# Kernel tuning notes

Measured on AMD Instinct MI355X. Metric: run time of the kernel, lower is better.

## Reference

```python
import jax, jax.numpy as jnp
import numpy as np

T, B, OBS, H, A = 128, 256, 128, 512, 18
LSTM_IN = H + A + 1  # trunk_out + one_hot(a) + r


def setup_inputs() -> dict:
    key = jax.random.key(0)
    ks = jax.random.split(key, 24)

    def rn(k, shape, scale=0.05):
        return jax.random.normal(k, shape, dtype=jnp.float32) * scale

    inp = {
        "o": jax.random.normal(ks[0], (T, B, OBS), dtype=jnp.float32),
        "a": jax.random.randint(ks[1], (T, B), 0, A, dtype=jnp.int32),
        "r": jax.random.normal(ks[2], (T, B), dtype=jnp.float32),
        "done": (jax.random.uniform(ks[3], (T, B)) < 0.05).astype(jnp.float32),
        "h0": jax.random.normal(ks[4], (B, H), dtype=jnp.float32) * 0.1,
        "c0": jax.random.normal(ks[5], (B, H), dtype=jnp.float32) * 0.1,
        # trunk
        "tW0": rn(ks[6], (OBS, H)), "tb0": jnp.zeros((H,), jnp.float32),
        "tW1": rn(ks[7], (H, H)), "tb1": jnp.zeros((H,), jnp.float32),
        # LSTM (PyTorch layout: gates stacked as [i, f, g, o])
        "W_ih": rn(ks[8], (4 * H, LSTM_IN)), "W_hh": rn(ks[9], (4 * H, H)),
        "b_ih": jnp.zeros((4 * H,), jnp.float32), "b_hh": jnp.zeros((4 * H,), jnp.float32),
        # advantage head
        "aW0": rn(ks[10], (H, H)), "ab0": jnp.zeros((H,), jnp.float32),
        "aW1": rn(ks[11], (H, A)), "ab1": jnp.zeros((A,), jnp.float32),
        # value head
        "vW0": rn(ks[12], (H, H)), "vb0": jnp.zeros((H,), jnp.float32),
        "vW1": rn(ks[13], (H, 1)), "vb1": jnp.zeros((1,), jnp.float32),
    }
    return inp


def _forward(o, a, r, done, h0, c0, tW0, tb0, tW1, tb1,
             W_ih, W_hh, b_ih, b_hh, aW0, ab0, aW1, ab1, vW0, vb0, vW1, vb1):
    # shared trunk: two Linear+ReLU layers, vectorized over T*B
    hidden = jax.nn.relu(jnp.einsum('tbi,ih->tbh', o, tW0) + tb0)
    hidden = jax.nn.relu(jnp.einsum('tbi,ih->tbh', hidden, tW1) + tb1)
    a_oh = jax.nn.one_hot(a, A, dtype=jnp.float32)          # [T,B,A]
    x = jnp.concatenate([hidden, r[..., None], a_oh], -1)    # [T,B,LSTM_IN]

    # precompute input projection for all steps (not state-dependent)
    xg = jnp.einsum('tbi,gi->tbg', x, W_ih) + b_ih + b_hh    # [T,B,4H]

    def step(carry, inp):
        h, c = carry
        xg_t, d_t = inp
        keep = (1.0 - d_t)[:, None]                          # per-step done reset
        h, c = h * keep, c * keep
        gates = xg_t + h @ W_hh.T                            # [B,4H]
        i, f, g, og = jnp.split(gates, 4, axis=-1)
        c = jax.nn.sigmoid(f) * c + jax.nn.sigmoid(i) * jnp.tanh(g)
        h = jax.nn.sigmoid(og) * jnp.tanh(c)
        return (h, c), h

    (hT, cT), hs = jax.lax.scan(step, (h0, c0), (xg, done))  # hs: [T,B,H]

    ah = jax.nn.relu(jnp.einsum('tbh,hk->tbk', hs, aW0) + ab0)
    adv = jnp.einsum('tbk,ka->tba', ah, aW1) + ab1            # [T,B,A]
    vh = jax.nn.relu(jnp.einsum('tbh,hk->tbk', hs, vW0) + vb0)
    val = jnp.einsum('tbk,kv->tbv', vh, vW1) + vb1            # [T,B,1]
    q = val + (adv - adv.mean(axis=-1, keepdims=True))
    return q, hT, cT


def reference(o, a, r, done, h0, c0, tW0, tb0, tW1, tb1,
              W_ih, W_hh, b_ih, b_hh, aW0, ab0, aW1, ab1, vW0, vb0, vW1, vb1):
    return _forward(o, a, r, done, h0, c0, tW0, tb0, tW1, tb1,
                    W_ih, W_hh, b_ih, b_hh, aW0, ab0, aW1, ab1, vW0, vb0, vW1, vb1)
```

## Files before the change

### kernel.cpp

```cpp
#include <hip/hip_runtime.h>
#include <cstdint>

typedef unsigned short u16;
typedef unsigned int u32;
typedef unsigned long long u64;
typedef float f32x4 __attribute__((ext_vector_type(4)));
typedef short s16x8 __attribute__((ext_vector_type(8)));

#define DEV static __device__ __forceinline__

#define TT 128
#define BB 256
#define OBSD 128
#define HHD 512
#define AD 18
#define GGD 2048
#define MMD 32768

DEV u16 f2bf(float f) {
  u32 u = __builtin_bit_cast(u32, f);
  u += 0x7fffu + ((u >> 16) & 1u);
  return (u16)(u >> 16);
}
DEV float bf2f(u16 h) { return __builtin_bit_cast(float, ((u32)h) << 16); }

DEV f32x4 mfma16x16x32(s16x8 a, s16x8 b, f32x4 c) {
  asm("v_mfma_f32_16x16x32_bf16 %0, %1, %2, %0" : "+v"(c) : "v"(a), "v"(b));
  return c;
}
DEV void fence_mfma_read(f32x4& x) { asm volatile("s_nop 7" : "+v"(x)); }
DEV void fence_mfma_srcc(f32x4& x) { asm volatile("s_nop 1" : "+v"(x)); }

typedef __attribute__((address_space(3))) char lds_char;
typedef __attribute__((address_space(1))) const char gl_char;
DEV void gload16(const char* g, char* l) {
  __builtin_amdgcn_global_load_lds((const gl_char*)g, (lds_char*)l, 16, 0, 0);
}

DEV float sigm(float x) { return 1.f / (1.f + __expf(-x)); }
DEV float tanh_fast(float x) {
  float t = __expf(-2.f * fabsf(x));
  float r = (1.f - t) / (1.f + t);
  return copysignf(r, x);
}

constexpr size_t OFF_FLAGS = 0;
constexpr size_t OFF_HRING = 524288;
constexpr size_t OFF_TW0T  = 1048576;
constexpr size_t OFF_TW1T  = 1179648;
constexpr size_t OFF_AW0T  = 1703936;
constexpr size_t OFF_VW0T  = 2228224;
constexpr size_t OFF_AW1T  = 2752512;
constexpr size_t OFF_VW1T  = 2770944;
constexpr size_t OFF_WIH   = 2772992;
constexpr size_t OFF_WHH   = 4870144;
constexpr size_t OFF_BSUM  = 6967296;
constexpr size_t OFF_WRC   = 6975488;
constexpr size_t OFF_WEMB  = 6983680;
constexpr size_t OFF_BCAT  = 7131136;
constexpr size_t OFF_OBF   = 8388608;
constexpr size_t OFF_BUF1  = 16777216;
constexpr size_t OFF_BUF2  = 50331648;
constexpr size_t OFF_BUF3  = 83886080;

__global__ __launch_bounds__(256) void prep(
    const float* __restrict__ o, const float* __restrict__ tW0,
    const float* __restrict__ tW1, const float* __restrict__ aW0,
    const float* __restrict__ vW0, const float* __restrict__ aW1,
    const float* __restrict__ vW1, const float* __restrict__ Wih,
    const float* __restrict__ WhhF, const float* __restrict__ bih,
    const float* __restrict__ bhh, const float* __restrict__ h0,
    const float* __restrict__ done, const float* __restrict__ ab0,
    const float* __restrict__ vb0,
    u16* __restrict__ o_bf, u16* __restrict__ tW0T, u16* __restrict__ tW1T,
    u16* __restrict__ aW0T, u16* __restrict__ vW0T, u16* __restrict__ aW1T,
    u16* __restrict__ vW1T, u16* __restrict__ WihB, u16* __restrict__ WhhB,
    float* __restrict__ bsum, float* __restrict__ wrc, float* __restrict__ wemb,
    float* __restrict__ bcat, u16* __restrict__ hring)
{
  const int total = 4178432;
  for (int id = blockIdx.x * 256 + threadIdx.x; id < total; id += gridDim.x * 256) {
    int i = id;
    if (i < 1048576) {
      float4 v = ((const float4*)o)[i];
      u16* dst = o_bf + (size_t)i * 4;
      dst[0] = f2bf(v.x); dst[1] = f2bf(v.y); dst[2] = f2bf(v.z); dst[3] = f2bf(v.w);
      continue;
    }
    i -= 1048576;
    if (i < 65536)  { int n = i >> 7, k = i & 127; tW0T[i] = f2bf(tW0[k * 512 + n]); continue; }
    i -= 65536;
    if (i < 262144) { int n = i >> 9, k = i & 511; tW1T[i] = f2bf(tW1[k * 512 + n]); continue; }
    i -= 262144;
    if (i < 262144) { int n = i >> 9, k = i & 511; aW0T[i] = f2bf(aW0[k * 512 + n]); continue; }
    i -= 262144;
    if (i < 262144) { int n = i >> 9, k = i & 511; vW0T[i] = f2bf(vW0[k * 512 + n]); continue; }
    i -= 262144;
    if (i < 9216)   { int n = i >> 9, k = i & 511; aW1T[i] = f2bf(aW1[k * 18 + n]); continue; }
    i -= 9216;
    if (i < 512)    { vW1T[i] = f2bf(vW1[i]); continue; }
    i -= 512;
    if (i < 1048576){ int g = i >> 9, k = i & 511; WihB[i] = f2bf(Wih[g * 531 + k]); continue; }
    i -= 1048576;
    if (i < 1048576){ WhhB[i] = f2bf(WhhF[i]); continue; }
    i -= 1048576;
    if (i < 2048)   { bsum[i] = bih[i] + bhh[i]; wrc[i] = Wih[i * 531 + 512]; continue; }
    i -= 2048;
    if (i < 36864)  { int j = i >> 11, g = i & 2047; wemb[i] = Wih[g * 531 + 513 + j]; continue; }
    i -= 36864;
    if (i < 1024)   { bcat[i] = (i < 512) ? ab0[i] : vb0[i - 512]; continue; }
    i -= 1024;
    { int b = i >> 9; hring[i] = f2bf(h0[i] * (1.f - done[b])); }
  }
}

template<int MODE>
__global__ __launch_bounds__(256) void gemm_bt(
    const u16* __restrict__ A, const u16* __restrict__ Bt, u16* __restrict__ C,
    int Mdim, int Ndim, int Kdim,
    const float* __restrict__ bias,
    const float* __restrict__ wrc, const float* __restrict__ wemb,
    const float* __restrict__ rin, const int* __restrict__ ain)
{
  __shared__ __align__(16) char smem[32768];
  const int tid = threadIdx.x;
  const int nTn = Ndim >> 7;
  int wg = blockIdx.x;
  {
    const int per = gridDim.x >> 3;
    wg = (wg & 7) * per + (wg >> 3);
  }
  const int tm = wg / nTn, tn = wg % nTn;
  const int wid = tid >> 6, lane = tid & 63;
  const int wr = wid >> 1, wc = wid & 1;
  const int l15 = lane & 15, l4 = lane >> 4;

  f32x4 acc[4][4];
#pragma unroll
  for (int i = 0; i < 4; ++i)
#pragma unroll
    for (int j = 0; j < 4; ++j) acc[i][j] = f32x4{0.f, 0.f, 0.f, 0.f};

  const int srow = lane >> 3;
  const int scolb = ((lane & 7) * 16) ^ (srow << 4);
  const size_t kd2 = (size_t)Kdim * 2;
  const char* Abase = (const char*)(A + (size_t)tm * 128 * Kdim);
  const char* Bbase = (const char*)(Bt + (size_t)tn * 128 * Kdim);
  const char* ga[4]; const char* gb[4]; char* la[4]; char* lb[4];
#pragma unroll
  for (int j = 0; j < 4; ++j) {
    const int row = wid * 32 + j * 8 + srow;
    ga[j] = Abase + (size_t)row * kd2 + scolb;
    gb[j] = Bbase + (size_t)row * kd2 + scolb;
    la[j] = smem + wid * 4096 + j * 1024;
    lb[j] = smem + 16384 + wid * 4096 + j * 1024;
  }

  for (int k0 = 0; k0 < Kdim; k0 += 64) {
    const size_t kb = (size_t)k0 * 2;
#pragma unroll
    for (int j = 0; j < 4; ++j) {
      gload16(ga[j] + kb, la[j]);
      gload16(gb[j] + kb, lb[j]);
    }
    __syncthreads();
#pragma unroll
    for (int kk = 0; kk < 2; ++kk) {
      s16x8 af[4], bfr[4];
#pragma unroll
      for (int i = 0; i < 4; ++i) {
        int ar = wr * 64 + i * 16 + l15;
        af[i] = *(const s16x8*)(smem + ((ar * 128 + kk * 64 + l4 * 16) ^ ((ar & 7) << 4)));
        int br = wc * 64 + i * 16 + l15;
        bfr[i] = *(const s16x8*)(smem + 16384 + ((br * 128 + kk * 64 + l4 * 16) ^ ((br & 7) << 4)));
      }
#pragma unroll
      for (int i = 0; i < 4; ++i)
#pragma unroll
        for (int j = 0; j < 4; ++j)
          acc[i][j] = mfma16x16x32(af[i], bfr[j], acc[i][j]);
    }
    __syncthreads();
  }

#pragma unroll
  for (int i = 0; i < 4; ++i)
#pragma unroll
    for (int j = 0; j < 4; ++j) fence_mfma_read(acc[i][j]);

#pragma unroll
  for (int i = 0; i < 4; ++i) {
    const int rowb = tm * 128 + wr * 64 + i * 16 + l4 * 4;
    float rv[4]; int av[4];
    if (MODE == 1) {
#pragma unroll
      for (int r = 0; r < 4; ++r) { rv[r] = rin[rowb + r]; av[r] = ain[rowb + r]; }
    }
#pragma unroll
    for (int j = 0; j < 4; ++j) {
      const int col = tn * 128 + wc * 64 + j * 16 + l15;
      const float bs = bias[col];
      if (MODE == 0) {
#pragma unroll
        for (int r = 0; r < 4; ++r) {
          float x = acc[i][j][r] + bs;
          x = fmaxf(x, 0.f);
          C[(size_t)(rowb + r) * Ndim + col] = f2bf(x);
        }
      } else {
        const float wcv = wrc[col];
#pragma unroll
        for (int r = 0; r < 4; ++r) {
          float x = acc[i][j][r] + bs + rv[r] * wcv + wemb[av[r] * GGD + col];
          C[(size_t)(rowb + r) * Ndim + col] = f2bf(x);
        }
      }
    }
  }
}

__global__ __launch_bounds__(256) void lstm_seq(
    const u16* __restrict__ xg, const u16* __restrict__ WhhB,
    const float* __restrict__ done, const float* __restrict__ c0,
    u16* __restrict__ hring, u16* __restrict__ hs,
    float* __restrict__ hT, float* __restrict__ cT, u32* __restrict__ cnt)
{
  __shared__ __align__(16) char wsm[65536];
  const int tid = threadIdx.x;
  const int bg = blockIdx.x & 3;
  const int ug = blockIdx.x >> 2;
  const int b0 = bg * 64;
  const int u0 = ug * 16;

#pragma unroll
  for (int i = 0; i < 16; ++i) {
    int idx = i * 256 + tid;
    int lr = idx >> 6, c8 = idx & 63;
    int g = lr >> 4, uu = lr & 15;
    uint4 v = *(const uint4*)(WhhB + (size_t)(g * 512 + u0 + uu) * 512 + c8 * 8);
    *(uint4*)(wsm + ((lr * 1024 + c8 * 16) ^ ((lr & 7) << 4))) = v;
  }
  __syncthreads();

  const int wid = tid >> 6, lane = tid & 63;
  const int l15 = lane & 15, l4 = lane >> 4;
  const int mrow = wid * 16 + l4 * 4;
  const int afrow = b0 + wid * 16 + l15;
  const int u = u0 + l15;
  u32* const mycnt = cnt + ((bg << 2) | wid) * TT;

  float creg[4], kc[4], kn[4];
#pragma unroll
  for (int r = 0; r < 4; ++r) {
    creg[r] = c0[(size_t)(b0 + mrow + r) * HHD + u];
    kc[r] = 1.f - done[b0 + mrow + r];
    kn[r] = 1.f - done[BB + b0 + mrow + r];
  }

  u16 xpf[16];
#pragma unroll
  for (int g = 0; g < 4; ++g)
#pragma unroll
    for (int r = 0; r < 4; ++r)
      xpf[g * 4 + r] = xg[(size_t)(b0 + mrow + r) * GGD + g * HHD + u];

  for (int t = 0; t < TT; ++t) {
    const u16* hsrc = hring + (size_t)(t & 1) * (BB * HHD);
    u16* hdst = hring + (size_t)((t + 1) & 1) * (BB * HHD);

    f32x4 acc[4];
#pragma unroll
    for (int g = 0; g < 4; ++g)
#pragma unroll
      for (int r = 0; r < 4; ++r)
        acc[g][r] = bf2f(xpf[g * 4 + r]);
#pragma unroll
    for (int g = 0; g < 4; ++g) fence_mfma_srcc(acc[g]);

    u64 aflo[16], afhi[16];
    const u64* hb = (const u64*)(hsrc + (size_t)afrow * HHD);
#pragma unroll
    for (int kk = 0; kk < 16; ++kk) {
      aflo[kk] = __hip_atomic_load(hb + kk * 8 + l4 * 2,
                                   __ATOMIC_RELAXED, __HIP_MEMORY_SCOPE_AGENT);
      afhi[kk] = __hip_atomic_load(hb + kk * 8 + l4 * 2 + 1,
                                   __ATOMIC_RELAXED, __HIP_MEMORY_SCOPE_AGENT);
    }
#pragma unroll
    for (int kk = 0; kk < 16; ++kk) {
      union { u64 q[2]; s16x8 v; } tmp;
      tmp.q[0] = aflo[kk]; tmp.q[1] = afhi[kk];
      s16x8 a = tmp.v;
#pragma unroll
      for (int g = 0; g < 4; ++g) {
        int br = g * 16 + l15;
        s16x8 b = *(const s16x8*)(wsm + ((br * 1024 + kk * 64 + l4 * 16) ^ ((br & 7) << 4)));
        acc[g] = mfma16x16x32(a, b, acc[g]);
      }
    }
#pragma unroll
    for (int g = 0; g < 4; ++g) fence_mfma_read(acc[g]);

    float hv_[4], cv_[4];
#pragma unroll
    for (int r = 0; r < 4; ++r) {
      float iv = sigm(acc[0][r]);
      float fv = sigm(acc[1][r]);
      float gv = tanh_fast(acc[2][r]);
      float ov = sigm(acc[3][r]);
      float c = fv * (creg[r] * kc[r]) + iv * gv;
      float h = ov * tanh_fast(c);
      creg[r] = c; cv_[r] = c; hv_[r] = h;
    }

    if (t < TT - 1) {
      u32 pw[4];
#pragma unroll
      for (int r = 0; r < 4; ++r) {
        u16 ob = f2bf(hv_[r] * kn[r]);
        u16 pb = (u16)__shfl_xor((int)ob, 1, 64);
        pw[r] = ((l15 & 1) == 0) ? ((u32)ob | ((u32)pb << 16))
                                 : ((u32)pb | ((u32)ob << 16));
      }
      {
        const int rb = (l15 & 1) * 2;
        u32* hd32 = (u32*)hdst;
        const int col2 = (u0 + (l15 & ~1)) >> 1;
        __hip_atomic_store(&hd32[(size_t)(b0 + mrow + rb) * 256 + col2], pw[rb],
                           __ATOMIC_RELAXED, __HIP_MEMORY_SCOPE_AGENT);
        __hip_atomic_store(&hd32[(size_t)(b0 + mrow + rb + 1) * 256 + col2], pw[rb + 1],
                           __ATOMIC_RELAXED, __HIP_MEMORY_SCOPE_AGENT);
      }
      asm volatile("s_waitcnt vmcnt(0)" ::: "memory");
      if (lane == 0)
        __hip_atomic_fetch_add(&mycnt[t], 1u,
                               __ATOMIC_RELAXED, __HIP_MEMORY_SCOPE_AGENT);
#pragma unroll
      for (int r = 0; r < 4; ++r)
        hs[((size_t)t * BB + b0 + mrow + r) * HHD + u] = f2bf(hv_[r]);
#pragma unroll
      for (int g = 0; g < 4; ++g)
#pragma unroll
        for (int r = 0; r < 4; ++r)
          xpf[g * 4 + r] = xg[((size_t)(t + 1) * BB + b0 + mrow + r) * GGD + g * HHD + u];
#pragma unroll
      for (int r = 0; r < 4; ++r) {
        kc[r] = kn[r];
        kn[r] = (t + 2 < TT) ? (1.f - done[(size_t)(t + 2) * BB + b0 + mrow + r]) : 1.f;
      }
      while (__hip_atomic_load(&mycnt[t],
                               __ATOMIC_RELAXED, __HIP_MEMORY_SCOPE_AGENT) < 32u)
        __builtin_amdgcn_s_sleep(1);
    } else {
#pragma unroll
      for (int r = 0; r < 4; ++r) {
        hs[((size_t)t * BB + b0 + mrow + r) * HHD + u] = f2bf(hv_[r]);
        hT[(size_t)(b0 + mrow + r) * HHD + u] = hv_[r];
        cT[(size_t)(b0 + mrow + r) * HHD + u] = cv_[r];
      }
    }
  }
}

__global__ __launch_bounds__(256) void head_final(
    const u16* __restrict__ hv, const u16* __restrict__ aW1T,
    const u16* __restrict__ vW1T, const float* __restrict__ ab1,
    const float* __restrict__ vb1, float* __restrict__ q)
{
  __shared__ __align__(16) u16 wa[AD * HHD];
  __shared__ __align__(16) u16 wv[HHD];
  const int tid = threadIdx.x;
  for (int i = tid; i < AD * HHD / 8; i += 256) ((uint4*)wa)[i] = ((const uint4*)aW1T)[i];
  for (int i = tid; i < HHD / 8; i += 256) ((uint4*)wv)[i] = ((const uint4*)vW1T)[i];
  __syncthreads();
  const int wid = tid >> 6, lane = tid & 63;
  for (int row = blockIdx.x * 4 + wid; row < MMD; row += gridDim.x * 4) {
    uint4 va = *(const uint4*)(hv + (size_t)row * 1024 + lane * 8);
    uint4 vv = *(const uint4*)(hv + (size_t)row * 1024 + 512 + lane * 8);
    const u16* pa = (const u16*)&va;
    const u16* pv = (const u16*)&vv;
    float af[8], vf[8];
#pragma unroll
    for (int j = 0; j < 8; ++j) { af[j] = bf2f(pa[j]); vf[j] = bf2f(pv[j]); }
    float accs[19];
#pragma unroll
    for (int n = 0; n < 19; ++n) accs[n] = 0.f;
#pragma unroll
    for (int n = 0; n < AD; ++n) {
      const u16* w = wa + n * HHD + lane * 8;
#pragma unroll
      for (int j = 0; j < 8; ++j) accs[n] += af[j] * bf2f(w[j]);
    }
    {
      const u16* w = wv + lane * 8;
#pragma unroll
      for (int j = 0; j < 8; ++j) accs[18] += vf[j] * bf2f(w[j]);
    }
#pragma unroll
    for (int n = 0; n < 19; ++n) {
#pragma unroll
      for (int off = 32; off > 0; off >>= 1)
        accs[n] += __shfl_xor(accs[n], off, 64);
    }
    if (lane == 0) {
      float s = 0.f;
      float advv[AD];
#pragma unroll
      for (int n = 0; n < AD; ++n) { advv[n] = accs[n] + ab1[n]; s += advv[n]; }
      float val = accs[18] + vb1[0];
      float mean = s * (1.f / 18.f);
#pragma unroll
      for (int n = 0; n < AD; ++n) q[(size_t)row * AD + n] = val + advv[n] - mean;
    }
  }
}

extern "C" void kernel_launch(void* const* d_in, const int* in_sizes, int n_in,
                              void* d_out, int out_size, void* d_ws, size_t ws_size,
                              hipStream_t stream) {
  const float* o    = (const float*)d_in[0];
  const int*   a    = (const int*)d_in[1];
  const float* r    = (const float*)d_in[2];
  const float* done = (const float*)d_in[3];
  const float* h0   = (const float*)d_in[4];
  const float* c0   = (const float*)d_in[5];
  const float* tW0  = (const float*)d_in[6];
  const float* tb0  = (const float*)d_in[7];
  const float* tW1  = (const float*)d_in[8];
  const float* tb1  = (const float*)d_in[9];
  const float* Wih  = (const float*)d_in[10];
  const float* Whh  = (const float*)d_in[11];
  const float* bih  = (const float*)d_in[12];
  const float* bhh  = (const float*)d_in[13];
  const float* aW0  = (const float*)d_in[14];
  const float* ab0  = (const float*)d_in[15];
  const float* aW1  = (const float*)d_in[16];
  const float* ab1  = (const float*)d_in[17];
  const float* vW0  = (const float*)d_in[18];
  const float* vb0  = (const float*)d_in[19];
  const float* vW1  = (const float*)d_in[20];
  const float* vb1  = (const float*)d_in[21];
  (void)in_sizes; (void)n_in; (void)ws_size;

  char* ws = (char*)d_ws;
  u32* cnt    = (u32*)(ws + OFF_FLAGS);
  u16* hring  = (u16*)(ws + OFF_HRING);
  u16* tW0T   = (u16*)(ws + OFF_TW0T);
  u16* tW1T   = (u16*)(ws + OFF_TW1T);
  u16* aW0T   = (u16*)(ws + OFF_AW0T);
  u16* vW0T   = (u16*)(ws + OFF_VW0T);
  u16* aW1T   = (u16*)(ws + OFF_AW1T);
  u16* vW1T   = (u16*)(ws + OFF_VW1T);
  u16* WihB   = (u16*)(ws + OFF_WIH);
  u16* WhhB   = (u16*)(ws + OFF_WHH);
  float* bsum = (float*)(ws + OFF_BSUM);
  float* wrc  = (float*)(ws + OFF_WRC);
  float* wemb = (float*)(ws + OFF_WEMB);
  float* bcat = (float*)(ws + OFF_BCAT);
  u16* o_bf   = (u16*)(ws + OFF_OBF);
  u16* buf1   = (u16*)(ws + OFF_BUF1);
  u16* buf2   = (u16*)(ws + OFF_BUF2);
  u16* buf3   = (u16*)(ws + OFF_BUF3);

  float* qout = (float*)d_out;
  float* hT   = qout + (size_t)TT * BB * AD;
  float* cT   = hT + (size_t)BB * HHD;

  hipMemsetAsync(cnt, 0, 65536, stream);
  prep<<<2048, 256, 0, stream>>>(o, tW0, tW1, aW0, vW0, aW1, vW1, Wih, Whh,
                                 bih, bhh, h0, done, ab0, vb0,
                                 o_bf, tW0T, tW1T, aW0T, vW0T, aW1T, vW1T,
                                 WihB, WhhB, bsum, wrc, wemb, bcat, hring);
  gemm_bt<0><<<1024, 256, 0, stream>>>(o_bf, tW0T, buf1, MMD, 512, 128, tb0,
                                       nullptr, nullptr, nullptr, nullptr);
  gemm_bt<0><<<1024, 256, 0, stream>>>(buf1, tW1T, buf2, MMD, 512, 512, tb1,
                                       nullptr, nullptr, nullptr, nullptr);
  gemm_bt<1><<<4096, 256, 0, stream>>>(buf2, WihB, buf3, MMD, 2048, 512, bsum,
                                       wrc, wemb, r, a);
  lstm_seq<<<128, 256, 0, stream>>>(buf3, WhhB, done, c0, hring,
                                    buf1 , hT, cT, cnt);
  gemm_bt<0><<<2048, 256, 0, stream>>>(buf1 , aW0T, buf3 , MMD, 1024, 512, bcat,
                                       nullptr, nullptr, nullptr, nullptr);
  head_final<<<2048, 256, 0, stream>>>(buf3, aW1T, vW1T, ab1, vb1, qout);
}
```

Measured before the change: 1.122 ms.

## Shrink LSTM grid to 32 blocks with per-row-group slot flags

The persistent LSTM kernel now runs on 32 blocks instead of 128. Each block owns 16 hidden units across all 256 batch rows, and each wave walks four row-group chunks per step. The single shared atomic counter per row group is replaced by per-producer slot flags, which a wave polls with a ballot before loading the previous h, and the xg prefetch moves ahead of the MFMA loop. The aim is to cut cross-block synchronization cost and let chunks pipeline, at the price of four times more serial work per block and fewer CUs in use.

```diff
diff --git a/kernel.cpp b/kernel.cpp
--- a/kernel.cpp
+++ b/kernel.cpp
@@ -219,17 +219,15 @@
   }
 }
 
-__global__ __launch_bounds__(256) void lstm_seq(
+__global__ __launch_bounds__(256, 1) void lstm_seq(
     const u16* __restrict__ xg, const u16* __restrict__ WhhB,
     const float* __restrict__ done, const float* __restrict__ c0,
     u16* __restrict__ hring, u16* __restrict__ hs,
-    float* __restrict__ hT, float* __restrict__ cT, u32* __restrict__ cnt)
+    float* __restrict__ hT, float* __restrict__ cT, u32* __restrict__ slots)
 {
   __shared__ __align__(16) char wsm[65536];
   const int tid = threadIdx.x;
-  const int bg = blockIdx.x & 3;
-  const int ug = blockIdx.x >> 2;
-  const int b0 = bg * 64;
+  const int ug = blockIdx.x;
   const int u0 = ug * 16;
 
 #pragma unroll
@@ -244,119 +242,140 @@
 
   const int wid = tid >> 6, lane = tid & 63;
   const int l15 = lane & 15, l4 = lane >> 4;
-  const int mrow = wid * 16 + l4 * 4;
-  const int afrow = b0 + wid * 16 + l15;
   const int u = u0 + l15;
-  u32* const mycnt = cnt + ((bg << 2) | wid) * TT;
-
-  float creg[4], kc[4], kn[4];
-#pragma unroll
-  for (int r = 0; r < 4; ++r) {
-    creg[r] = c0[(size_t)(b0 + mrow + r) * HHD + u];
-    kc[r] = 1.f - done[b0 + mrow + r];
-    kn[r] = 1.f - done[BB + b0 + mrow + r];
-  }
-
-  u16 xpf[16];
-#pragma unroll
-  for (int g = 0; g < 4; ++g)
-#pragma unroll
-    for (int r = 0; r < 4; ++r)
-      xpf[g * 4 + r] = xg[(size_t)(b0 + mrow + r) * GGD + g * HHD + u];
+
+  float creg[4][4], kc[4][4], kn[4][4];
+  u16 xpf[4][16];
+#pragma unroll
+  for (int ch = 0; ch < 4; ++ch) {
+    const int b0 = (ch * 4 + wid) * 16;
+#pragma unroll
+    for (int r = 0; r < 4; ++r) {
+      const int row = b0 + l4 * 4 + r;
+      creg[ch][r] = c0[(size_t)row * HHD + u];
+      kc[ch][r] = 1.f - done[row];
+      kn[ch][r] = 1.f - done[BB + row];
+    }
+#pragma unroll
+    for (int g = 0; g < 4; ++g)
+#pragma unroll
+      for (int r = 0; r < 4; ++r)
+        xpf[ch][g * 4 + r] = xg[(size_t)(b0 + l4 * 4 + r) * GGD + g * HHD + u];
+  }
 
   for (int t = 0; t < TT; ++t) {
     const u16* hsrc = hring + (size_t)(t & 1) * (BB * HHD);
     u16* hdst = hring + (size_t)((t + 1) & 1) * (BB * HHD);
 
-    f32x4 acc[4];
-#pragma unroll
-    for (int g = 0; g < 4; ++g)
-#pragma unroll
-      for (int r = 0; r < 4; ++r)
-        acc[g][r] = bf2f(xpf[g * 4 + r]);
-#pragma unroll
-    for (int g = 0; g < 4; ++g) fence_mfma_srcc(acc[g]);
-
-    u64 aflo[16], afhi[16];
-    const u64* hb = (const u64*)(hsrc + (size_t)afrow * HHD);
-#pragma unroll
-    for (int kk = 0; kk < 16; ++kk) {
-      aflo[kk] = __hip_atomic_load(hb + kk * 8 + l4 * 2,
-                                   __ATOMIC_RELAXED, __HIP_MEMORY_SCOPE_AGENT);
-      afhi[kk] = __hip_atomic_load(hb + kk * 8 + l4 * 2 + 1,
-                                   __ATOMIC_RELAXED, __HIP_MEMORY_SCOPE_AGENT);
-    }
-#pragma unroll
-    for (int kk = 0; kk < 16; ++kk) {
-      union { u64 q[2]; s16x8 v; } tmp;
-      tmp.q[0] = aflo[kk]; tmp.q[1] = afhi[kk];
-      s16x8 a = tmp.v;
-#pragma unroll
-      for (int g = 0; g < 4; ++g) {
-        int br = g * 16 + l15;
-        s16x8 b = *(const s16x8*)(wsm + ((br * 1024 + kk * 64 + l4 * 16) ^ ((br & 7) << 4)));
-        acc[g] = mfma16x16x32(a, b, acc[g]);
-      }
-    }
-#pragma unroll
-    for (int g = 0; g < 4; ++g) fence_mfma_read(acc[g]);
-
-    float hv_[4], cv_[4];
-#pragma unroll
-    for (int r = 0; r < 4; ++r) {
-      float iv = sigm(acc[0][r]);
-      float fv = sigm(acc[1][r]);
-      float gv = tanh_fast(acc[2][r]);
-      float ov = sigm(acc[3][r]);
-      float c = fv * (creg[r] * kc[r]) + iv * gv;
-      float h = ov * tanh_fast(c);
-      creg[r] = c; cv_[r] = c; hv_[r] = h;
-    }
-
-    if (t < TT - 1) {
-      u32 pw[4];
+#pragma unroll
+    for (int ch = 0; ch < 4; ++ch) {
+      const int rg = ch * 4 + wid;
+      const int b0 = rg * 16;
+      const int mrow = l4 * 4;
+
+      if (t > 0) {
+        for (;;) {
+          u32 v = 1;
+          if (lane < 32)
+            v = __hip_atomic_load(&slots[((size_t)rg * TT + (t - 1)) * 32 + lane],
+                                  __ATOMIC_RELAXED, __HIP_MEMORY_SCOPE_AGENT);
+          if (__all(v != 0)) break;
+          __builtin_amdgcn_s_sleep(1);
+        }
+      }
+
+      u64 aflo[16], afhi[16];
+      const u64* hb = (const u64*)(hsrc + (size_t)(b0 + l15) * HHD);
+#pragma unroll
+      for (int kk = 0; kk < 16; ++kk) {
+        aflo[kk] = __hip_atomic_load(hb + kk * 8 + l4 * 2,
+                                     __ATOMIC_RELAXED, __HIP_MEMORY_SCOPE_AGENT);
+        afhi[kk] = __hip_atomic_load(hb + kk * 8 + l4 * 2 + 1,
+                                     __ATOMIC_RELAXED, __HIP_MEMORY_SCOPE_AGENT);
+      }
+
+      f32x4 acc[4];
+#pragma unroll
+      for (int g = 0; g < 4; ++g)
+#pragma unroll
+        for (int r = 0; r < 4; ++r)
+          acc[g][r] = bf2f(xpf[ch][g * 4 + r]);
+#pragma unroll
+      for (int g = 0; g < 4; ++g) fence_mfma_srcc(acc[g]);
+
+      if (t < TT - 1) {
+#pragma unroll
+        for (int g = 0; g < 4; ++g)
+#pragma unroll
+          for (int r = 0; r < 4; ++r)
+            xpf[ch][g * 4 + r] =
+                xg[((size_t)(t + 1) * BB + b0 + mrow + r) * GGD + g * HHD + u];
+      }
+
+#pragma unroll
+      for (int kk = 0; kk < 16; ++kk) {
+        union { u64 q[2]; s16x8 v; } tmp;
+        tmp.q[0] = aflo[kk]; tmp.q[1] = afhi[kk];
+        s16x8 a = tmp.v;
+#pragma unroll
+        for (int g = 0; g < 4; ++g) {
+          int br = g * 16 + l15;
+          s16x8 b = *(const s16x8*)(wsm + ((br * 1024 + kk * 64 + l4 * 16) ^ ((br & 7) << 4)));
+          acc[g] = mfma16x16x32(a, b, acc[g]);
+        }
+      }
+#pragma unroll
+      for (int g = 0; g < 4; ++g) fence_mfma_read(acc[g]);
+
+      float hv_[4], cv_[4];
 #pragma unroll
       for (int r = 0; r < 4; ++r) {
-        u16 ob = f2bf(hv_[r] * kn[r]);
-        u16 pb = (u16)__shfl_xor((int)ob, 1, 64);
-        pw[r] = ((l15 & 1) == 0) ? ((u32)ob | ((u32)pb << 16))
-                                 : ((u32)pb | ((u32)ob << 16));
-      }
-      {
-        const int rb = (l15 & 1) * 2;
-        u32* hd32 = (u32*)hdst;
-        const int col2 = (u0 + (l15 & ~1)) >> 1;
-        __hip_atomic_store(&hd32[(size_t)(b0 + mrow + rb) * 256 + col2], pw[rb],
-                           __ATOMIC_RELAXED, __HIP_MEMORY_SCOPE_AGENT);
-        __hip_atomic_store(&hd32[(size_t)(b0 + mrow + rb + 1) * 256 + col2], pw[rb + 1],
-                           __ATOMIC_RELAXED, __HIP_MEMORY_SCOPE_AGENT);
-      }
-      asm volatile("s_waitcnt vmcnt(0)" ::: "memory");
-      if (lane == 0)
-        __hip_atomic_fetch_add(&mycnt[t], 1u,
-                               __ATOMIC_RELAXED, __HIP_MEMORY_SCOPE_AGENT);
-#pragma unroll
-      for (int r = 0; r < 4; ++r)
-        hs[((size_t)t * BB + b0 + mrow + r) * HHD + u] = f2bf(hv_[r]);
-#pragma unroll
-      for (int g = 0; g < 4; ++g)
+        float iv = sigm(acc[0][r]);
+        float fv = sigm(acc[1][r]);
+        float gv = tanh_fast(acc[2][r]);
+        float ov = sigm(acc[3][r]);
+        float c = fv * (creg[ch][r] * kc[ch][r]) + iv * gv;
+        float h = ov * tanh_fast(c);
+        creg[ch][r] = c; cv_[r] = c; hv_[r] = h;
+      }
+
+      if (t < TT - 1) {
 #pragma unroll
         for (int r = 0; r < 4; ++r)
-          xpf[g * 4 + r] = xg[((size_t)(t + 1) * BB + b0 + mrow + r) * GGD + g * HHD + u];
-#pragma unroll
-      for (int r = 0; r < 4; ++r) {
-        kc[r] = kn[r];
-        kn[r] = (t + 2 < TT) ? (1.f - done[(size_t)(t + 2) * BB + b0 + mrow + r]) : 1.f;
-      }
-      while (__hip_atomic_load(&mycnt[t],
-                               __ATOMIC_RELAXED, __HIP_MEMORY_SCOPE_AGENT) < 32u)
-        __builtin_amdgcn_s_sleep(1);
-    } else {
-#pragma unroll
-      for (int r = 0; r < 4; ++r) {
-        hs[((size_t)t * BB + b0 + mrow + r) * HHD + u] = f2bf(hv_[r]);
-        hT[(size_t)(b0 + mrow + r) * HHD + u] = hv_[r];
-        cT[(size_t)(b0 + mrow + r) * HHD + u] = cv_[r];
+          hs[((size_t)t * BB + b0 + mrow + r) * HHD + u] = f2bf(hv_[r]);
+        u32 pw[4];
+#pragma unroll
+        for (int r = 0; r < 4; ++r) {
+          u16 ob = f2bf(hv_[r] * kn[ch][r]);
+          u16 pb = (u16)__shfl_xor((int)ob, 1, 64);
+          pw[r] = ((l15 & 1) == 0) ? ((u32)ob | ((u32)pb << 16))
+                                   : ((u32)pb | ((u32)ob << 16));
+        }
+        {
+          const int rb = (l15 & 1) * 2;
+          u32* hd32 = (u32*)hdst;
+          const int col2 = (u0 + (l15 & ~1)) >> 1;
+          __hip_atomic_store(&hd32[(size_t)(b0 + mrow + rb) * 256 + col2], pw[rb],
+                             __ATOMIC_RELAXED, __HIP_MEMORY_SCOPE_AGENT);
+          __hip_atomic_store(&hd32[(size_t)(b0 + mrow + rb + 1) * 256 + col2], pw[rb + 1],
+                             __ATOMIC_RELAXED, __HIP_MEMORY_SCOPE_AGENT);
+        }
+        asm volatile("s_waitcnt vmcnt(0)" ::: "memory");
+        if (lane == 0)
+          __hip_atomic_store(&slots[((size_t)rg * TT + t) * 32 + ug], 1u,
+                             __ATOMIC_RELAXED, __HIP_MEMORY_SCOPE_AGENT);
+#pragma unroll
+        for (int r = 0; r < 4; ++r) {
+          kc[ch][r] = kn[ch][r];
+          kn[ch][r] = (t + 2 < TT) ? (1.f - done[(size_t)(t + 2) * BB + b0 + mrow + r]) : 1.f;
+        }
+      } else {
+#pragma unroll
+        for (int r = 0; r < 4; ++r) {
+          hs[((size_t)t * BB + b0 + mrow + r) * HHD + u] = f2bf(hv_[r]);
+          hT[(size_t)(b0 + mrow + r) * HHD + u] = hv_[r];
+          cT[(size_t)(b0 + mrow + r) * HHD + u] = cv_[r];
+        }
       }
     }
   }
@@ -443,7 +462,7 @@
   (void)in_sizes; (void)n_in; (void)ws_size;
 
   char* ws = (char*)d_ws;
-  u32* cnt    = (u32*)(ws + OFF_FLAGS);
+  u32* slots  = (u32*)(ws + OFF_FLAGS);
   u16* hring  = (u16*)(ws + OFF_HRING);
   u16* tW0T   = (u16*)(ws + OFF_TW0T);
   u16* tW1T   = (u16*)(ws + OFF_TW1T);
@@ -466,7 +485,7 @@
   float* hT   = qout + (size_t)TT * BB * AD;
   float* cT   = hT + (size_t)BB * HHD;
 
-  hipMemsetAsync(cnt, 0, 65536, stream);
+  hipMemsetAsync(slots, 0, 262144, stream);
   prep<<<2048, 256, 0, stream>>>(o, tW0, tW1, aW0, vW0, aW1, vW1, Wih, Whh,
                                  bih, bhh, h0, done, ab0, vb0,
                                  o_bf, tW0T, tW1T, aW0T, vW0T, aW1T, vW1T,
@@ -477,8 +496,8 @@
                                        nullptr, nullptr, nullptr, nullptr);
   gemm_bt<1><<<4096, 256, 0, stream>>>(buf2, WihB, buf3, MMD, 2048, 512, bsum,
                                        wrc, wemb, r, a);
-  lstm_seq<<<128, 256, 0, stream>>>(buf3, WhhB, done, c0, hring,
-                                    buf1 , hT, cT, cnt);
+  lstm_seq<<<32, 256, 0, stream>>>(buf3, WhhB, done, c0, hring,
+                                   buf1 , hT, cT, slots);
   gemm_bt<0><<<2048, 256, 0, stream>>>(buf1 , aW0T, buf3 , MMD, 1024, 512, bcat,
                                        nullptr, nullptr, nullptr, nullptr);
   head_final<<<2048, 256, 0, stream>>>(buf3, aW1T, vW1T, ab1, vb1, qout);
```

After: 3.943 ms. +251.4%, slower.

## Fuse head first-layer GEMM into LSTM recurrence using idle per-step compute

Applied to the files above, without the earlier changes.

Moves the advantage/value head's first Linear+ReLU into the persistent LSTM kernel. Each step it multiplies the previous step's h fragments, already held in registers, by a 32-column slice of the head weights kept in LDS, and writes the ah/vh outputs directly. This removes the separate head GEMM launch and the hs write/read round trip. Done-masking moves from scaling h at store time to masking the A-fragments at load, so the unmasked h can be reused by the head. The trade-off is extra MFMA work, 32KB more LDS per block, and more stores on the latency-critical serial path.

```diff
diff --git a/kernel.cpp b/kernel.cpp
--- a/kernel.cpp
+++ b/kernel.cpp
@@ -30,6 +30,7 @@
 }
 DEV void fence_mfma_read(f32x4& x) { asm volatile("s_nop 7" : "+v"(x)); }
 DEV void fence_mfma_srcc(f32x4& x) { asm volatile("s_nop 1" : "+v"(x)); }
+DEV void fence_valu_srca(s16x8& x) { asm volatile("s_nop 1" : "+v"(x)); }
 
 typedef __attribute__((address_space(3))) char lds_char;
 typedef __attribute__((address_space(1))) const char gl_char;
@@ -70,8 +71,7 @@
     const float* __restrict__ vW1, const float* __restrict__ Wih,
     const float* __restrict__ WhhF, const float* __restrict__ bih,
     const float* __restrict__ bhh, const float* __restrict__ h0,
-    const float* __restrict__ done, const float* __restrict__ ab0,
-    const float* __restrict__ vb0,
+    const float* __restrict__ ab0, const float* __restrict__ vb0,
     u16* __restrict__ o_bf, u16* __restrict__ tW0T, u16* __restrict__ tW1T,
     u16* __restrict__ aW0T, u16* __restrict__ vW0T, u16* __restrict__ aW1T,
     u16* __restrict__ vW1T, u16* __restrict__ WihB, u16* __restrict__ WhhB,
@@ -110,7 +110,7 @@
     i -= 36864;
     if (i < 1024)   { bcat[i] = (i < 512) ? ab0[i] : vb0[i - 512]; continue; }
     i -= 1024;
-    { int b = i >> 9; hring[i] = f2bf(h0[i] * (1.f - done[b])); }
+    { hring[i] = f2bf(h0[i]); }
   }
 }
 
@@ -219,18 +219,21 @@
   }
 }
 
-__global__ __launch_bounds__(256) void lstm_seq(
+__global__ __launch_bounds__(256, 1) void lstm_seq(
     const u16* __restrict__ xg, const u16* __restrict__ WhhB,
-    const float* __restrict__ done, const float* __restrict__ c0,
-    u16* __restrict__ hring, u16* __restrict__ hs,
+    const u16* __restrict__ WheadT, const float* __restrict__ done,
+    const float* __restrict__ c0, const float* __restrict__ bcat,
+    u16* __restrict__ hring, u16* __restrict__ ah, u16* __restrict__ vh,
     float* __restrict__ hT, float* __restrict__ cT, u32* __restrict__ cnt)
 {
   __shared__ __align__(16) char wsm[65536];
+  __shared__ __align__(16) char whd[32768];
   const int tid = threadIdx.x;
   const int bg = blockIdx.x & 3;
   const int ug = blockIdx.x >> 2;
   const int b0 = bg * 64;
   const int u0 = ug * 16;
+  const int hc0 = ug * 32;
 
 #pragma unroll
   for (int i = 0; i < 16; ++i) {
@@ -240,6 +243,13 @@
     uint4 v = *(const uint4*)(WhhB + (size_t)(g * 512 + u0 + uu) * 512 + c8 * 8);
     *(uint4*)(wsm + ((lr * 1024 + c8 * 16) ^ ((lr & 7) << 4))) = v;
   }
+#pragma unroll
+  for (int i = 0; i < 8; ++i) {
+    int idx = i * 256 + tid;
+    int lr = idx >> 6, c8 = idx & 63;
+    uint4 v = *(const uint4*)(WheadT + (size_t)(hc0 + lr) * 512 + c8 * 8);
+    *(uint4*)(whd + ((lr * 1024 + c8 * 16) ^ ((lr & 7) << 4))) = v;
+  }
   __syncthreads();
 
   const int wid = tid >> 6, lane = tid & 63;
@@ -249,13 +259,20 @@
   const int u = u0 + l15;
   u32* const mycnt = cnt + ((bg << 2) | wid) * TT;
 
-  float creg[4], kc[4], kn[4];
+  u16* const hvout = (ug < 16) ? ah : vh;
+  const int hcl = (ug < 16) ? hc0 : hc0 - 512;
+  float bcv[2];
+#pragma unroll
+  for (int j = 0; j < 2; ++j) bcv[j] = bcat[hc0 + j * 16 + l15];
+
+  float creg[4], kc[4];
 #pragma unroll
   for (int r = 0; r < 4; ++r) {
     creg[r] = c0[(size_t)(b0 + mrow + r) * HHD + u];
     kc[r] = 1.f - done[b0 + mrow + r];
-    kn[r] = 1.f - done[BB + b0 + mrow + r];
-  }
+  }
+  u64 am;
+  { float dn = done[afrow]; am = (dn != 0.f) ? 0ull : ~0ull; }
 
   u16 xpf[16];
 #pragma unroll
@@ -289,8 +306,9 @@
 #pragma unroll
     for (int kk = 0; kk < 16; ++kk) {
       union { u64 q[2]; s16x8 v; } tmp;
-      tmp.q[0] = aflo[kk]; tmp.q[1] = afhi[kk];
+      tmp.q[0] = aflo[kk] & am; tmp.q[1] = afhi[kk] & am;
       s16x8 a = tmp.v;
+      fence_valu_srca(a);
 #pragma unroll
       for (int g = 0; g < 4; ++g) {
         int br = g * 16 + l15;
@@ -313,59 +331,129 @@
       creg[r] = c; cv_[r] = c; hv_[r] = h;
     }
 
-    if (t < TT - 1) {
+    {
       u32 pw[4];
 #pragma unroll
       for (int r = 0; r < 4; ++r) {
-        u16 ob = f2bf(hv_[r] * kn[r]);
+        u16 ob = f2bf(hv_[r]);
         u16 pb = (u16)__shfl_xor((int)ob, 1, 64);
         pw[r] = ((l15 & 1) == 0) ? ((u32)ob | ((u32)pb << 16))
                                  : ((u32)pb | ((u32)ob << 16));
       }
-      {
-        const int rb = (l15 & 1) * 2;
-        u32* hd32 = (u32*)hdst;
-        const int col2 = (u0 + (l15 & ~1)) >> 1;
-        __hip_atomic_store(&hd32[(size_t)(b0 + mrow + rb) * 256 + col2], pw[rb],
-                           __ATOMIC_RELAXED, __HIP_MEMORY_SCOPE_AGENT);
-        __hip_atomic_store(&hd32[(size_t)(b0 + mrow + rb + 1) * 256 + col2], pw[rb + 1],
-                           __ATOMIC_RELAXED, __HIP_MEMORY_SCOPE_AGENT);
-      }
-      asm volatile("s_waitcnt vmcnt(0)" ::: "memory");
-      if (lane == 0)
-        __hip_atomic_fetch_add(&mycnt[t], 1u,
-                               __ATOMIC_RELAXED, __HIP_MEMORY_SCOPE_AGENT);
-#pragma unroll
-      for (int r = 0; r < 4; ++r)
-        hs[((size_t)t * BB + b0 + mrow + r) * HHD + u] = f2bf(hv_[r]);
+      const int rb = (l15 & 1) * 2;
+      u32* hd32 = (u32*)hdst;
+      const int col2 = (u0 + (l15 & ~1)) >> 1;
+      __hip_atomic_store(&hd32[(size_t)(b0 + mrow + rb) * 256 + col2], pw[rb],
+                         __ATOMIC_RELAXED, __HIP_MEMORY_SCOPE_AGENT);
+      __hip_atomic_store(&hd32[(size_t)(b0 + mrow + rb + 1) * 256 + col2], pw[rb + 1],
+                         __ATOMIC_RELAXED, __HIP_MEMORY_SCOPE_AGENT);
+    }
+    asm volatile("s_waitcnt vmcnt(0)" ::: "memory");
+    if (lane == 0)
+      __hip_atomic_fetch_add(&mycnt[t], 1u,
+                             __ATOMIC_RELAXED, __HIP_MEMORY_SCOPE_AGENT);
+
+    if (t > 0) {
+      f32x4 acch[2];
+#pragma unroll
+      for (int j = 0; j < 2; ++j)
+#pragma unroll
+        for (int r = 0; r < 4; ++r) acch[j][r] = bcv[j];
+#pragma unroll
+      for (int j = 0; j < 2; ++j) fence_mfma_srcc(acch[j]);
+#pragma unroll
+      for (int kk = 0; kk < 16; ++kk) {
+        union { u64 q[2]; s16x8 v; } tmp;
+        tmp.q[0] = aflo[kk]; tmp.q[1] = afhi[kk];
+        s16x8 a = tmp.v;
+#pragma unroll
+        for (int j = 0; j < 2; ++j) {
+          int br = j * 16 + l15;
+          s16x8 b = *(const s16x8*)(whd + ((br * 1024 + kk * 64 + l4 * 16) ^ ((br & 7) << 4)));
+          acch[j] = mfma16x16x32(a, b, acch[j]);
+        }
+      }
+#pragma unroll
+      for (int j = 0; j < 2; ++j) fence_mfma_read(acch[j]);
+#pragma unroll
+      for (int j = 0; j < 2; ++j)
+#pragma unroll
+        for (int r = 0; r < 4; ++r) {
+          float x = fmaxf(acch[j][r], 0.f);
+          hvout[((size_t)(t - 1) * BB + b0 + mrow + r) * 512 + hcl + j * 16 + l15] = f2bf(x);
+        }
+    }
+    if (t == TT - 1) {
+#pragma unroll
+      for (int r = 0; r < 4; ++r) {
+        hT[(size_t)(b0 + mrow + r) * HHD + u] = hv_[r];
+        cT[(size_t)(b0 + mrow + r) * HHD + u] = cv_[r];
+      }
+    } else {
 #pragma unroll
       for (int g = 0; g < 4; ++g)
 #pragma unroll
         for (int r = 0; r < 4; ++r)
           xpf[g * 4 + r] = xg[((size_t)(t + 1) * BB + b0 + mrow + r) * GGD + g * HHD + u];
 #pragma unroll
+      for (int r = 0; r < 4; ++r)
+        kc[r] = 1.f - done[(size_t)(t + 1) * BB + b0 + mrow + r];
+      float dn = done[(size_t)(t + 1) * BB + afrow];
+      am = (dn != 0.f) ? 0ull : ~0ull;
+    }
+
+    while (__hip_atomic_load(&mycnt[t],
+                             __ATOMIC_RELAXED, __HIP_MEMORY_SCOPE_AGENT) < 32u)
+      __builtin_amdgcn_s_sleep(1);
+  }
+
+  {
+    const u16* hfin = hring + (size_t)(TT & 1) * (BB * HHD);
+    u64 aflo[16], afhi[16];
+    const u64* hb = (const u64*)(hfin + (size_t)afrow * HHD);
+#pragma unroll
+    for (int kk = 0; kk < 16; ++kk) {
+      aflo[kk] = __hip_atomic_load(hb + kk * 8 + l4 * 2,
+                                   __ATOMIC_RELAXED, __HIP_MEMORY_SCOPE_AGENT);
+      afhi[kk] = __hip_atomic_load(hb + kk * 8 + l4 * 2 + 1,
+                                   __ATOMIC_RELAXED, __HIP_MEMORY_SCOPE_AGENT);
+    }
+    f32x4 acch[2];
+#pragma unroll
+    for (int j = 0; j < 2; ++j)
+#pragma unroll
+      for (int r = 0; r < 4; ++r) acch[j][r] = bcv[j];
+#pragma unroll
+    for (int j = 0; j < 2; ++j) fence_mfma_srcc(acch[j]);
+#pragma unroll
+    for (int kk = 0; kk < 16; ++kk) {
+      union { u64 q[2]; s16x8 v; } tmp;
+      tmp.q[0] = aflo[kk]; tmp.q[1] = afhi[kk];
+      s16x8 a = tmp.v;
+#pragma unroll
+      for (int j = 0; j < 2; ++j) {
+        int br = j * 16 + l15;
+        s16x8 b = *(const s16x8*)(whd + ((br * 1024 + kk * 64 + l4 * 16) ^ ((br & 7) << 4)));
+        acch[j] = mfma16x16x32(a, b, acch[j]);
+      }
+    }
+#pragma unroll
+    for (int j = 0; j < 2; ++j) fence_mfma_read(acch[j]);
+#pragma unroll
+    for (int j = 0; j < 2; ++j)
+#pragma unroll
       for (int r = 0; r < 4; ++r) {
-        kc[r] = kn[r];
-        kn[r] = (t + 2 < TT) ? (1.f - done[(size_t)(t + 2) * BB + b0 + mrow + r]) : 1.f;
-      }
-      while (__hip_atomic_load(&mycnt[t],
-                               __ATOMIC_RELAXED, __HIP_MEMORY_SCOPE_AGENT) < 32u)
-        __builtin_amdgcn_s_sleep(1);
-    } else {
-#pragma unroll
-      for (int r = 0; r < 4; ++r) {
-        hs[((size_t)t * BB + b0 + mrow + r) * HHD + u] = f2bf(hv_[r]);
-        hT[(size_t)(b0 + mrow + r) * HHD + u] = hv_[r];
-        cT[(size_t)(b0 + mrow + r) * HHD + u] = cv_[r];
-      }
-    }
+        float x = fmaxf(acch[j][r], 0.f);
+        hvout[((size_t)(TT - 1) * BB + b0 + mrow + r) * 512 + hcl + j * 16 + l15] = f2bf(x);
+      }
   }
 }
 
 __global__ __launch_bounds__(256) void head_final(
-    const u16* __restrict__ hv, const u16* __restrict__ aW1T,
-    const u16* __restrict__ vW1T, const float* __restrict__ ab1,
-    const float* __restrict__ vb1, float* __restrict__ q)
+    const u16* __restrict__ ah, const u16* __restrict__ vh,
+    const u16* __restrict__ aW1T, const u16* __restrict__ vW1T,
+    const float* __restrict__ ab1, const float* __restrict__ vb1,
+    float* __restrict__ q)
 {
   __shared__ __align__(16) u16 wa[AD * HHD];
   __shared__ __align__(16) u16 wv[HHD];
@@ -375,8 +463,8 @@
   __syncthreads();
   const int wid = tid >> 6, lane = tid & 63;
   for (int row = blockIdx.x * 4 + wid; row < MMD; row += gridDim.x * 4) {
-    uint4 va = *(const uint4*)(hv + (size_t)row * 1024 + lane * 8);
-    uint4 vv = *(const uint4*)(hv + (size_t)row * 1024 + 512 + lane * 8);
+    uint4 va = *(const uint4*)(ah + (size_t)row * 512 + lane * 8);
+    uint4 vv = *(const uint4*)(vh + (size_t)row * 512 + lane * 8);
     const u16* pa = (const u16*)&va;
     const u16* pv = (const u16*)&vv;
     float af[8], vf[8];
@@ -468,7 +556,7 @@
 
   hipMemsetAsync(cnt, 0, 65536, stream);
   prep<<<2048, 256, 0, stream>>>(o, tW0, tW1, aW0, vW0, aW1, vW1, Wih, Whh,
-                                 bih, bhh, h0, done, ab0, vb0,
+                                 bih, bhh, h0, ab0, vb0,
                                  o_bf, tW0T, tW1T, aW0T, vW0T, aW1T, vW1T,
                                  WihB, WhhB, bsum, wrc, wemb, bcat, hring);
   gemm_bt<0><<<1024, 256, 0, stream>>>(o_bf, tW0T, buf1, MMD, 512, 128, tb0,
@@ -477,9 +565,7 @@
                                        nullptr, nullptr, nullptr, nullptr);
   gemm_bt<1><<<4096, 256, 0, stream>>>(buf2, WihB, buf3, MMD, 2048, 512, bsum,
                                        wrc, wemb, r, a);
-  lstm_seq<<<128, 256, 0, stream>>>(buf3, WhhB, done, c0, hring,
-                                    buf1 , hT, cT, cnt);
-  gemm_bt<0><<<2048, 256, 0, stream>>>(buf1 , aW0T, buf3 , MMD, 1024, 512, bcat,
-                                       nullptr, nullptr, nullptr, nullptr);
-  head_final<<<2048, 256, 0, stream>>>(buf3, aW1T, vW1T, ab1, vb1, qout);
-}
+  lstm_seq<<<128, 256, 0, stream>>>(buf3, WhhB, aW0T, done, c0, bcat, hring,
+                                    buf1 , buf2 , hT, cT, cnt);
+  head_final<<<2048, 256, 0, stream>>>(buf1, buf2, aW1T, vW1T, ab1, vb1, qout);
+}
```

Result: faster. 1.012 ms, median of 2 (-9.8%).
